# Kernel optimization log

Hardware: AMD Instinct MI355X
Metric: run time of the kernel (lower is better)

## Reference

```python
import jax, jax.numpy as jnp
import numpy as np


def setup_inputs() -> dict:
    key = jax.random.key(0)
    ks = jax.random.split(key, 6)
    B, H, T, Dk, Dv = 64, 16, 4, 128, 256
    q = jax.random.normal(ks[0], (B, H, T, Dk), dtype=jnp.float32)
    k = jax.random.normal(ks[1], (B, H, T, Dk), dtype=jnp.float32)
    v = jax.random.normal(ks[2], (B, H, T, Dv), dtype=jnp.float32)
    g = jax.random.uniform(ks[3], (B, H, T), dtype=jnp.float32)
    beta = jax.random.uniform(ks[4], (B, H, T), dtype=jnp.float32)
    last_recurrent_state = jax.random.normal(ks[5], (B, H, Dk, Dv), dtype=jnp.float32)
    return {"q": q, "k": k, "v": v, "g": g, "beta": beta,
            "last_recurrent_state": last_recurrent_state}


def reference(q, k, v, g, beta, last_recurrent_state):
    # q,k: (B,H,T,Dk)  v: (B,H,T,Dv)  g,beta: (B,H,T)  state: (B,H,Dk,Dv)
    def step(state, xs):
        q_t, k_t, v_t, g_t, beta_t = xs  # (B,H,Dk),(B,H,Dk),(B,H,Dv),(B,H),(B,H)
        state = state * jnp.exp(g_t)[..., None, None]           # decay
        kv_mem = jnp.einsum('bhkv,bhk->bhv', state, k_t)         # readout with key
        delta = (v_t - kv_mem) * beta_t[..., None]               # delta-rule correction
        state = state + k_t[..., None] * delta[..., None, :]     # rank-1 update
        out_t = jnp.einsum('bhkv,bhk->bhv', state, q_t)          # query readout
        return state, out_t

    xs = (jnp.moveaxis(q, 2, 0), jnp.moveaxis(k, 2, 0), jnp.moveaxis(v, 2, 0),
          jnp.moveaxis(g, 2, 0), jnp.moveaxis(beta, 2, 0))
    state, outs = jax.lax.scan(step, last_recurrent_state, xs)
    output = jnp.moveaxis(outs, 0, 2)  # (B,H,T,Dv)
    return jnp.concatenate([output.reshape(-1), state.reshape(-1)], axis=0)
```

## Files before the change

### kernel.cpp

```cpp
#include <hip/hip_runtime.h>

#define BH    1024
#define TT    4
#define DK    128
#define DV    256
#define KSEG  16
#define KLEN  8
#define QV    64
#define LDP   9

typedef float vfloat4 __attribute__((ext_vector_type(4)));

__global__ __launch_bounds__(256)
void delta_rule_kernel(const float* __restrict__ q,
                       const float* __restrict__ k,
                       const float* __restrict__ v,
                       const float* __restrict__ g,
                       const float* __restrict__ beta,
                       const float* __restrict__ s0,
                       float* __restrict__ out)
{
    const int bh      = blockIdx.x >> 2;
    const int quarter = blockIdx.x & 3;
    const int tid  = threadIdx.x;
    const int kg   = tid & (KSEG - 1);
    const int vg   = tid >> 4;
    const int vcol = quarter * QV + vg * 4;
    const int kr0  = kg * KLEN;

    const float* __restrict__ sin_p = s0 + (size_t)bh * DK * DV;
    float* __restrict__ out_p  = out + (size_t)bh * TT * DV;
    float* __restrict__ sout_p = out + (size_t)BH * TT * DV + (size_t)bh * DK * DV;

    const float* __restrict__ kbase = k    + (size_t)bh * TT * DK;
    const float* __restrict__ qbase = q    + (size_t)bh * TT * DK;
    const float* __restrict__ vbase = v    + (size_t)bh * TT * DV;
    const float* __restrict__ gbase = g    + (size_t)bh * TT;
    const float* __restrict__ bbase = beta + (size_t)bh * TT;

    __shared__ float ks[TT][KSEG * LDP];
    __shared__ float qs[TT][KSEG * LDP];

    const int i0 = tid;
    const int i1 = tid + 256;
    const float kl0 = kbase[i0];
    const float kl1 = kbase[i1];
    const float ql0 = qbase[i0];
    const float ql1 = qbase[i1];

    const float4 gq = *(const float4*)&gbase[0];
    const float4 bq = *(const float4*)&bbase[0];
    float4 v4a[TT];
#pragma unroll
    for (int t = 0; t < TT; ++t)
        v4a[t] = *(const float4*)&vbase[t * DV + vcol];

    float4 s4[KLEN];
#pragma unroll
    for (int kk = 0; kk < KLEN; ++kk)
        s4[kk] = *(const float4*)&sin_p[(size_t)(kr0 + kk) * DV + vcol];

    {
        const int t0 = i0 >> 7, j0 = i0 & 127;
        const int t1 = i1 >> 7, j1 = i1 & 127;
        ks[t0][(j0 >> 3) * LDP + (j0 & 7)] = kl0;
        ks[t1][(j1 >> 3) * LDP + (j1 & 7)] = kl1;
        qs[t0][(j0 >> 3) * LDP + (j0 & 7)] = ql0;
        qs[t1][(j1 >> 3) * LDP + (j1 & 7)] = ql1;
    }
    __syncthreads();

    const float garr[TT] = {gq.x, gq.y, gq.z, gq.w};
    const float barr[TT] = {bq.x, bq.y, bq.z, bq.w};

#pragma unroll
    for (int t = 0; t < TT; ++t) {
        const float gt = expf(garr[t]);
        const float bt = barr[t];
        const float4 v4 = v4a[t];

        float4 kv = make_float4(0.f, 0.f, 0.f, 0.f);
#pragma unroll
        for (int kk = 0; kk < KLEN; ++kk) {
            const float kt = ks[t][kg * LDP + kk];
            s4[kk].x *= gt; s4[kk].y *= gt; s4[kk].z *= gt; s4[kk].w *= gt;
            kv.x = fmaf(s4[kk].x, kt, kv.x);
            kv.y = fmaf(s4[kk].y, kt, kv.y);
            kv.z = fmaf(s4[kk].z, kt, kv.z);
            kv.w = fmaf(s4[kk].w, kt, kv.w);
        }
#pragma unroll
        for (int m = 1; m < KSEG; m <<= 1) {
            kv.x += __shfl_xor(kv.x, m);
            kv.y += __shfl_xor(kv.y, m);
            kv.z += __shfl_xor(kv.z, m);
            kv.w += __shfl_xor(kv.w, m);
        }

        float4 d4;
        d4.x = (v4.x - kv.x) * bt;
        d4.y = (v4.y - kv.y) * bt;
        d4.z = (v4.z - kv.z) * bt;
        d4.w = (v4.w - kv.w) * bt;

        float4 o4 = make_float4(0.f, 0.f, 0.f, 0.f);
#pragma unroll
        for (int kk = 0; kk < KLEN; ++kk) {
            const float kt = ks[t][kg * LDP + kk];
            const float qt = qs[t][kg * LDP + kk];
            s4[kk].x = fmaf(kt, d4.x, s4[kk].x);
            s4[kk].y = fmaf(kt, d4.y, s4[kk].y);
            s4[kk].z = fmaf(kt, d4.z, s4[kk].z);
            s4[kk].w = fmaf(kt, d4.w, s4[kk].w);
            o4.x = fmaf(s4[kk].x, qt, o4.x);
            o4.y = fmaf(s4[kk].y, qt, o4.y);
            o4.z = fmaf(s4[kk].z, qt, o4.z);
            o4.w = fmaf(s4[kk].w, qt, o4.w);
        }
#pragma unroll
        for (int m = 1; m < KSEG; m <<= 1) {
            o4.x += __shfl_xor(o4.x, m);
            o4.y += __shfl_xor(o4.y, m);
            o4.z += __shfl_xor(o4.z, m);
            o4.w += __shfl_xor(o4.w, m);
        }
        if (kg == 0) {
            vfloat4 ov = { o4.x, o4.y, o4.z, o4.w };
            __builtin_nontemporal_store(ov, (vfloat4*)&out_p[t * DV + vcol]);
        }
    }

#pragma unroll
    for (int kk = 0; kk < KLEN; ++kk) {
        vfloat4 sv = { s4[kk].x, s4[kk].y, s4[kk].z, s4[kk].w };
        __builtin_nontemporal_store(sv,
            (vfloat4*)&sout_p[(size_t)(kr0 + kk) * DV + vcol]);
    }
}

extern "C" void kernel_launch(void* const* d_in, const int* in_sizes, int n_in,
                              void* d_out, int out_size, void* d_ws, size_t ws_size,
                              hipStream_t stream) {
    const float* q    = (const float*)d_in[0];
    const float* k    = (const float*)d_in[1];
    const float* v    = (const float*)d_in[2];
    const float* g    = (const float*)d_in[3];
    const float* beta = (const float*)d_in[4];
    const float* s0   = (const float*)d_in[5];
    float* out = (float*)d_out;

    delta_rule_kernel<<<dim3(BH * 4), dim3(256), 0, stream>>>(q, k, v, g, beta, s0, out);
}
```

Measured before the change: 276.1 us.

## Process full head per block with cross-wave LDS reduction instead of shuffles

Each block now handles an entire (b,h) state: the four waves each own 32 key rows, and each lane owns 4 value columns across all 256 columns. The per-step kv and output reductions, previously done with intra-wave xor shuffles over 16 key segments, now go through shared-memory buffers with block barriers. This cuts shuffle traffic and quarters the number of blocks so k/q/v/g/beta are loaded once per head rather than four times. In exchange each thread holds 128 state floats in registers, which raises register pressure and lowers occupancy on a memory-bound kernel. It also adds a barrier per step and drops the nontemporal stores.

After: 252.9 us. 8.4% less time.

```diff
diff --git a/kernel.cpp b/kernel.cpp
--- a/kernel.cpp
+++ b/kernel.cpp
@@ -4,12 +4,8 @@
 #define TT    4
 #define DK    128
 #define DV    256
-#define KSEG  16
-#define KLEN  8
-#define QV    64
-#define LDP   9
-
-typedef float vfloat4 __attribute__((ext_vector_type(4)));
+#define NW    4
+#define RPW   32
 
 __global__ __launch_bounds__(256)
 void delta_rule_kernel(const float* __restrict__ q,
@@ -20,13 +16,12 @@
                        const float* __restrict__ s0,
                        float* __restrict__ out)
 {
-    const int bh      = blockIdx.x >> 2;
-    const int quarter = blockIdx.x & 3;
-    const int tid  = threadIdx.x;
-    const int kg   = tid & (KSEG - 1);
-    const int vg   = tid >> 4;
-    const int vcol = quarter * QV + vg * 4;
-    const int kr0  = kg * KLEN;
+    const int bh  = blockIdx.x;
+    const int tid = threadIdx.x;
+    const int w   = tid >> 6;
+    const int l   = tid & 63;
+    const int col = l << 2;
+    const int r0  = w * RPW;
 
     const float* __restrict__ sin_p = s0 + (size_t)bh * DK * DV;
     float* __restrict__ out_p  = out + (size_t)bh * TT * DV;
@@ -38,35 +33,34 @@
     const float* __restrict__ gbase = g    + (size_t)bh * TT;
     const float* __restrict__ bbase = beta + (size_t)bh * TT;
 
-    __shared__ float ks[TT][KSEG * LDP];
-    __shared__ float qs[TT][KSEG * LDP];
+    __shared__ float ks[TT][DK];
+    __shared__ float qs[TT][DK];
+    __shared__ float kvbuf[TT][NW][DV];
+    __shared__ float obuf [TT][NW][DV];
 
-    const int i0 = tid;
-    const int i1 = tid + 256;
-    const float kl0 = kbase[i0];
-    const float kl1 = kbase[i1];
-    const float ql0 = qbase[i0];
-    const float ql1 = qbase[i1];
+    const float kl0 = kbase[tid];
+    const float kl1 = kbase[tid + 256];
+    const float ql0 = qbase[tid];
+    const float ql1 = qbase[tid + 256];
 
     const float4 gq = *(const float4*)&gbase[0];
     const float4 bq = *(const float4*)&bbase[0];
     float4 v4a[TT];
 #pragma unroll
     for (int t = 0; t < TT; ++t)
-        v4a[t] = *(const float4*)&vbase[t * DV + vcol];
+        v4a[t] = *(const float4*)&vbase[t * DV + col];
 
-    float4 s4[KLEN];
+    float4 s4[RPW];
 #pragma unroll
-    for (int kk = 0; kk < KLEN; ++kk)
-        s4[kk] = *(const float4*)&sin_p[(size_t)(kr0 + kk) * DV + vcol];
+    for (int i = 0; i < RPW; ++i)
+        s4[i] = *(const float4*)&sin_p[(size_t)(r0 + i) * DV + col];
 
+    ks[tid >> 7][tid & 127] = kl0;
+    qs[tid >> 7][tid & 127] = ql0;
     {
-        const int t0 = i0 >> 7, j0 = i0 & 127;
-        const int t1 = i1 >> 7, j1 = i1 & 127;
-        ks[t0][(j0 >> 3) * LDP + (j0 & 7)] = kl0;
-        ks[t1][(j1 >> 3) * LDP + (j1 & 7)] = kl1;
-        qs[t0][(j0 >> 3) * LDP + (j0 & 7)] = ql0;
-        qs[t1][(j1 >> 3) * LDP + (j1 & 7)] = ql1;
+        const int j = tid + 256;
+        ks[j >> 7][j & 127] = kl1;
+        qs[j >> 7][j & 127] = ql1;
     }
     __syncthreads();
 
@@ -77,64 +71,78 @@
     for (int t = 0; t < TT; ++t) {
         const float gt = expf(garr[t]);
         const float bt = barr[t];
-        const float4 v4 = v4a[t];
 
         float4 kv = make_float4(0.f, 0.f, 0.f, 0.f);
 #pragma unroll
-        for (int kk = 0; kk < KLEN; ++kk) {
-            const float kt = ks[t][kg * LDP + kk];
-            s4[kk].x *= gt; s4[kk].y *= gt; s4[kk].z *= gt; s4[kk].w *= gt;
-            kv.x = fmaf(s4[kk].x, kt, kv.x);
-            kv.y = fmaf(s4[kk].y, kt, kv.y);
-            kv.z = fmaf(s4[kk].z, kt, kv.z);
-            kv.w = fmaf(s4[kk].w, kt, kv.w);
+        for (int j = 0; j < RPW / 4; ++j) {
+            const float4 k4 = *(const float4*)&ks[t][r0 + 4 * j];
+            const float ka[4] = {k4.x, k4.y, k4.z, k4.w};
+#pragma unroll
+            for (int rr = 0; rr < 4; ++rr) {
+                float4& s = s4[4 * j + rr];
+                const float kr = ka[rr];
+                s.x *= gt; s.y *= gt; s.z *= gt; s.w *= gt;
+                kv.x = fmaf(s.x, kr, kv.x);
+                kv.y = fmaf(s.y, kr, kv.y);
+                kv.z = fmaf(s.z, kr, kv.z);
+                kv.w = fmaf(s.w, kr, kv.w);
+            }
         }
+        *(float4*)&kvbuf[t][w][col] = kv;
+        __syncthreads();
+
+        const float4 p0 = *(const float4*)&kvbuf[t][0][col];
+        const float4 p1 = *(const float4*)&kvbuf[t][1][col];
+        const float4 p2 = *(const float4*)&kvbuf[t][2][col];
+        const float4 p3 = *(const float4*)&kvbuf[t][3][col];
+        float4 d;
+        d.x = (v4a[t].x - (p0.x + p1.x + p2.x + p3.x)) * bt;
+        d.y = (v4a[t].y - (p0.y + p1.y + p2.y + p3.y)) * bt;
+        d.z = (v4a[t].z - (p0.z + p1.z + p2.z + p3.z)) * bt;
+        d.w = (v4a[t].w - (p0.w + p1.w + p2.w + p3.w)) * bt;
+
+        float4 o = make_float4(0.f, 0.f, 0.f, 0.f);
 #pragma unroll
-        for (int m = 1; m < KSEG; m <<= 1) {
-            kv.x += __shfl_xor(kv.x, m);
-            kv.y += __shfl_xor(kv.y, m);
-            kv.z += __shfl_xor(kv.z, m);
-            kv.w += __shfl_xor(kv.w, m);
+        for (int j = 0; j < RPW / 4; ++j) {
+            const float4 k4 = *(const float4*)&ks[t][r0 + 4 * j];
+            const float4 q4 = *(const float4*)&qs[t][r0 + 4 * j];
+            const float ka[4] = {k4.x, k4.y, k4.z, k4.w};
+            const float qa[4] = {q4.x, q4.y, q4.z, q4.w};
+#pragma unroll
+            for (int rr = 0; rr < 4; ++rr) {
+                float4& s = s4[4 * j + rr];
+                const float kr = ka[rr];
+                const float qr = qa[rr];
+                s.x = fmaf(kr, d.x, s.x);
+                s.y = fmaf(kr, d.y, s.y);
+                s.z = fmaf(kr, d.z, s.z);
+                s.w = fmaf(kr, d.w, s.w);
+                o.x = fmaf(s.x, qr, o.x);
+                o.y = fmaf(s.y, qr, o.y);
+                o.z = fmaf(s.z, qr, o.z);
+                o.w = fmaf(s.w, qr, o.w);
+            }
         }
-
-        float4 d4;
-        d4.x = (v4.x - kv.x) * bt;
-        d4.y = (v4.y - kv.y) * bt;
-        d4.z = (v4.z - kv.z) * bt;
-        d4.w = (v4.w - kv.w) * bt;
-
-        float4 o4 = make_float4(0.f, 0.f, 0.f, 0.f);
-#pragma unroll
-        for (int kk = 0; kk < KLEN; ++kk) {
-            const float kt = ks[t][kg * LDP + kk];
-            const float qt = qs[t][kg * LDP + kk];
-            s4[kk].x = fmaf(kt, d4.x, s4[kk].x);
-            s4[kk].y = fmaf(kt, d4.y, s4[kk].y);
-            s4[kk].z = fmaf(kt, d4.z, s4[kk].z);
-            s4[kk].w = fmaf(kt, d4.w, s4[kk].w);
-            o4.x = fmaf(s4[kk].x, qt, o4.x);
-            o4.y = fmaf(s4[kk].y, qt, o4.y);
-            o4.z = fmaf(s4[kk].z, qt, o4.z);
-            o4.w = fmaf(s4[kk].w, qt, o4.w);
-        }
-#pragma unroll
-        for (int m = 1; m < KSEG; m <<= 1) {
-            o4.x += __shfl_xor(o4.x, m);
-            o4.y += __shfl_xor(o4.y, m);
-            o4.z += __shfl_xor(o4.z, m);
-            o4.w += __shfl_xor(o4.w, m);
-        }
-        if (kg == 0) {
-            vfloat4 ov = { o4.x, o4.y, o4.z, o4.w };
-            __builtin_nontemporal_store(ov, (vfloat4*)&out_p[t * DV + vcol]);
-        }
+        *(float4*)&obuf[t][w][col] = o;
     }
 
 #pragma unroll
-    for (int kk = 0; kk < KLEN; ++kk) {
-        vfloat4 sv = { s4[kk].x, s4[kk].y, s4[kk].z, s4[kk].w };
-        __builtin_nontemporal_store(sv,
-            (vfloat4*)&sout_p[(size_t)(kr0 + kk) * DV + vcol]);
+    for (int i = 0; i < RPW; ++i)
+        *(float4*)&sout_p[(size_t)(r0 + i) * DV + col] = s4[i];
+
+    __syncthreads();
+
+    {
+        const float4 a0 = *(const float4*)&obuf[w][0][col];
+        const float4 a1 = *(const float4*)&obuf[w][1][col];
+        const float4 a2 = *(const float4*)&obuf[w][2][col];
+        const float4 a3 = *(const float4*)&obuf[w][3][col];
+        float4 oo;
+        oo.x = a0.x + a1.x + a2.x + a3.x;
+        oo.y = a0.y + a1.y + a2.y + a3.y;
+        oo.z = a0.z + a1.z + a2.z + a3.z;
+        oo.w = a0.w + a1.w + a2.w + a3.w;
+        *(float4*)&out_p[w * DV + col] = oo;
     }
 }
 
@@ -149,5 +157,5 @@
     const float* s0   = (const float*)d_in[5];
     float* out = (float*)d_out;
 
-    delta_rule_kernel<<<dim3(BH * 4), dim3(256), 0, stream>>>(q, k, v, g, beta, s0, out);
+    delta_rule_kernel<<<dim3(BH), dim3(256), 0, stream>>>(q, k, v, g, beta, s0, out);
 }
```
